# Kernel optimization log

Measured on AMD Instinct MI355X. Metric: run time of the kernel, lower is better.

Reference implementation:

```python
import jax, jax.numpy as jnp
import numpy as np

SEQ, BATCH, HID, OUT = 2048, 128, 256, 2

def setup_inputs() -> dict:
    key = jax.random.key(0)
    ks = jax.random.split(key, 6)
    return {
        "x": jax.random.normal(ks[0], (SEQ, BATCH), dtype=jnp.float32),
        # torch code draws h inside forward: randn*0.01 + 0.5 -> pass as input for determinism
        "h0": jax.random.normal(ks[1], (BATCH, HID), dtype=jnp.float32) * 0.01 + 0.5,
        "W_ih": jax.random.normal(ks[2], (HID, 1), dtype=jnp.float32) * 0.05 + 0.4,
        "W_hh": jax.random.normal(ks[3], (HID, HID), dtype=jnp.float32) * 0.2,
        "W_hh_bias": jax.random.normal(ks[4], (HID, HID), dtype=jnp.float32) * 0.01 + 0.5,
        "b_h": jnp.zeros((HID,), dtype=jnp.float32),
        "W": jax.random.normal(ks[5], (OUT, HID), dtype=jnp.float32) * 0.1 + 0.5,
        "b": jnp.zeros((OUT,), dtype=jnp.float32),
        "context": 1,
    }

def reference(x, h0, W_ih, W_hh, W_hh_bias, b_h, W, b, context):
    # context is a scalar, so c1 + c2 = (2h-1) @ (W_hh + context*W_hh_bias).T (same math, one GEMM)
    W_eff = W_hh + context * W_hh_bias            # (hid, hid)
    w_in = W_ih[:, 0]                             # input_size == 1 -> (hid,)

    def step(h, x_t):
        # c0: (batch,1)@(1,hid) == outer product of x_t with W_ih column
        pre = x_t[:, None] * w_in[None, :] + (2.0 * h - 1.0) @ W_eff.T + b_h
        h_new = jax.nn.sigmoid(pre)
        return h_new, h_new

    _, hs = jax.lax.scan(step, h0, x)             # hs: (seq, batch, hid)
    out = jnp.transpose(hs, (1, 0, 2))            # (batch, seq, hid)
    y = out @ W.T + b                             # (batch, seq, out)
    return y[:, :, 0], out
```

## Files before the change

kernel.cpp:

```cpp
#include <hip/hip_runtime.h>
#include <math.h>

#define SEQ   2048
#define BATCH 128
#define HID   256
#define NCH   16
#define KCH   16
#define VST   20

template <int CTRL>
__device__ __forceinline__ float dpp_mov(float x) {
    return __int_as_float(__builtin_amdgcn_update_dpp(
        __float_as_int(x), __float_as_int(x), CTRL, 0xF, 0xF, false));
}

__global__ __launch_bounds__(512, 2)
void rnn_scan_kernel(const float* __restrict__ x,
                     const float* __restrict__ h0,
                     const float* __restrict__ W_ih,
                     const float* __restrict__ W_hh,
                     const float* __restrict__ W_hh_b,
                     const float* __restrict__ b_h,
                     const int*   __restrict__ context,
                     float*       __restrict__ out_hs)
{
    const int b   = blockIdx.x;
    const int tid = threadIdx.x;
    const int R   = tid >> 4;
    const int l   = tid & 15;
    const int l7  = tid & 7;
    const int row = 8 * R + l7;

    __shared__ __align__(16) float v_lds[2][NCH * VST];
    __shared__ float x_lds[SEQ];

    for (int t = tid; t < SEQ; t += 512)
        x_lds[t] = x[t * BATCH + b];

    const float ctx = (float)context[0];

    float4 wreg[8][4];
    #pragma unroll
    for (int j = 0; j < 8; ++j) {
        const int rj = 8 * R + (l7 ^ j);
        const float* wp = W_hh   + (size_t)rj * HID + KCH * l;
        const float* bp = W_hh_b + (size_t)rj * HID + KCH * l;
        #pragma unroll
        for (int c = 0; c < 4; ++c) {
            const float4 a = *(const float4*)(wp + 4 * c);
            const float4 d = *(const float4*)(bp + 4 * c);
            wreg[j][c] = make_float4(a.x + ctx * d.x, a.y + ctx * d.y,
                                     a.z + ctx * d.z, a.w + ctx * d.w);
        }
    }

    const float winj = W_ih[row];
    const float bhj  = b_h[row];

    const int voff = VST * (row >> 4) + (row & 15);
    v_lds[0][voff] = 2.f * h0[(size_t)b * HID + row] - 1.f;

    float* outp = out_hs + (size_t)b * SEQ * HID + row;

    const float4* vr0 = (const float4*)(v_lds[0] + VST * l);
    const float4* vr1 = (const float4*)(v_lds[1] + VST * l);

    __syncthreads();

    auto step = [&](int t, const float4* __restrict__ vr, float* __restrict__ vw) {
        float q[8] = {0.f, 0.f, 0.f, 0.f, 0.f, 0.f, 0.f, 0.f};
        #pragma unroll
        for (int c = 0; c < 4; ++c) {
            const float4 v4 = vr[c];
            #pragma unroll
            for (int j = 0; j < 8; ++j) {
                const float4 w = wreg[j][c];
                q[j] += w.x * v4.x;
                q[j] += w.y * v4.y;
                q[j] += w.z * v4.z;
                q[j] += w.w * v4.w;
            }
        }
        #pragma unroll
        for (int j = 0; j < 8; ++j) q[j] += dpp_mov<0x128>(q[j]);
        q[0] += dpp_mov<0xB1>(q[1]);
        q[2] += dpp_mov<0xB1>(q[3]);
        q[4] += dpp_mov<0xB1>(q[5]);
        q[6] += dpp_mov<0xB1>(q[7]);
        q[0] += dpp_mov<0x4E>(q[2]);
        q[4] += dpp_mov<0x4E>(q[6]);
        q[0] += dpp_mov<0x124>(q[4]);

        const float pre = q[0] + bhj + x_lds[t] * winj;
        const float h = __builtin_amdgcn_rcpf(1.f + __expf(-pre));
        vw[voff] = 2.f * h - 1.f;
        if ((tid & 8) == 0)
            outp[(size_t)t * HID] = h;
        __syncthreads();
    };

    for (int t = 0; t < SEQ; t += 2) {
        step(t,     vr0, v_lds[1]);
        step(t + 1, vr1, v_lds[0]);
    }
}

__global__ __launch_bounds__(256, 4)
void head_kernel(const float* __restrict__ hs,
                 const float* __restrict__ W,
                 const float* __restrict__ bias,
                 float*       __restrict__ y)
{
    const int tid  = threadIdx.x;
    const int lane = tid & 63;
    const int sub  = lane & 15;
    const int rsub = lane >> 4;

    float4 w0[4];
    #pragma unroll
    for (int u = 0; u < 4; ++u)
        w0[u] = *(const float4*)(W + 4 * (16 * u + sub));
    const float b0 = bias[0];

    const int gwave = (blockIdx.x * blockDim.x + tid) >> 6;
    const int nw    = (gridDim.x * blockDim.x) >> 6;
    const int nq    = (BATCH * SEQ) >> 2;

    for (int q = gwave; q < nq; q += nw) {
        const int rrow = q * 4 + rsub;
        const float* rp = hs + (size_t)rrow * HID;
        float s = 0.f;
        #pragma unroll
        for (int u = 0; u < 4; ++u) {
            const float4 hv = *(const float4*)(rp + 4 * (16 * u + sub));
            s += hv.x * w0[u].x + hv.y * w0[u].y +
                 hv.z * w0[u].z + hv.w * w0[u].w;
        }
        s += __shfl_xor(s, 1, 64);
        s += __shfl_xor(s, 2, 64);
        s += __shfl_xor(s, 4, 64);
        s += __shfl_xor(s, 8, 64);
        if (sub == 0) y[rrow] = s + b0;
    }
}

extern "C" void kernel_launch(void* const* d_in, const int* in_sizes, int n_in,
                              void* d_out, int out_size, void* d_ws, size_t ws_size,
                              hipStream_t stream) {
    const float* x      = (const float*)d_in[0];
    const float* h0     = (const float*)d_in[1];
    const float* W_ih   = (const float*)d_in[2];
    const float* W_hh   = (const float*)d_in[3];
    const float* W_hh_b = (const float*)d_in[4];
    const float* b_h    = (const float*)d_in[5];
    const float* W      = (const float*)d_in[6];
    const float* bias   = (const float*)d_in[7];
    const int*   ctx    = (const int*)d_in[8];

    float* y  = (float*)d_out;
    float* hs = y + (size_t)BATCH * SEQ;

    rnn_scan_kernel<<<BATCH, 512, 0, stream>>>(x, h0, W_ih, W_hh, W_hh_b,
                                               b_h, ctx, hs);
    head_kernel<<<2048, 256, 0, stream>>>(hs, W, bias, y);
}
```

Before: 1.470 ms.

## Fuse output head projection into RNN scan kernel epilogue

Removes the separate head kernel and has each scan block compute y for its own batch row after the recurrence finishes, reading back the hs it just wrote. This drops one kernel launch and lets the head work run per block without a second grid. In exchange the head runs on only 128 blocks, so bandwidth use is lower, and it adds a threadfence. It also changes the sigmoid reciprocal from rcpf to a full divide, changes the launch-bounds attribute to waves_per_eu, and hoists the x_lds load to the top of the step.

```diff
diff --git a/kernel.cpp b/kernel.cpp
--- a/kernel.cpp
+++ b/kernel.cpp
@@ -14,7 +14,7 @@
         __float_as_int(x), __float_as_int(x), CTRL, 0xF, 0xF, false));
 }
 
-__global__ __launch_bounds__(512, 2)
+__global__ __launch_bounds__(512) __attribute__((amdgpu_waves_per_eu(2, 2)))
 void rnn_scan_kernel(const float* __restrict__ x,
                      const float* __restrict__ h0,
                      const float* __restrict__ W_ih,
@@ -22,7 +22,10 @@
                      const float* __restrict__ W_hh_b,
                      const float* __restrict__ b_h,
                      const int*   __restrict__ context,
-                     float*       __restrict__ out_hs)
+                     const float* __restrict__ Wout,
+                     const float* __restrict__ bias,
+                     float*       __restrict__ out_hs,
+                     float*       __restrict__ out_y)
 {
     const int b   = blockIdx.x;
     const int tid = threadIdx.x;
@@ -68,6 +71,7 @@
     __syncthreads();
 
     auto step = [&](int t, const float4* __restrict__ vr, float* __restrict__ vw) {
+        const float xt = x_lds[t];
         float q[8] = {0.f, 0.f, 0.f, 0.f, 0.f, 0.f, 0.f, 0.f};
         #pragma unroll
         for (int c = 0; c < 4; ++c) {
@@ -91,8 +95,8 @@
         q[4] += dpp_mov<0x4E>(q[6]);
         q[0] += dpp_mov<0x124>(q[4]);
 
-        const float pre = q[0] + bhj + x_lds[t] * winj;
-        const float h = __builtin_amdgcn_rcpf(1.f + __expf(-pre));
+        const float pre = q[0] + bhj + xt * winj;
+        const float h = 1.f / (1.f + __expf(-pre));
         vw[voff] = 2.f * h - 1.f;
         if ((tid & 8) == 0)
             outp[(size_t)t * HID] = h;
@@ -103,44 +107,37 @@
         step(t,     vr0, v_lds[1]);
         step(t + 1, vr1, v_lds[0]);
     }
-}
 
-__global__ __launch_bounds__(256, 4)
-void head_kernel(const float* __restrict__ hs,
-                 const float* __restrict__ W,
-                 const float* __restrict__ bias,
-                 float*       __restrict__ y)
-{
-    const int tid  = threadIdx.x;
-    const int lane = tid & 63;
-    const int sub  = lane & 15;
-    const int rsub = lane >> 4;
+    __threadfence();
+    __syncthreads();
 
-    float4 w0[4];
-    #pragma unroll
-    for (int u = 0; u < 4; ++u)
-        w0[u] = *(const float4*)(W + 4 * (16 * u + sub));
-    const float b0 = bias[0];
+    {
+        const int sub  = tid & 15;
+        const int rsub = tid >> 4;
+        float4 w0[4];
+        #pragma unroll
+        for (int u = 0; u < 4; ++u)
+            w0[u] = *(const float4*)(Wout + 4 * (16 * u + sub));
+        const float b0 = bias[0];
+        const float* hsb = out_hs + (size_t)b * SEQ * HID;
+        float* yp = out_y + (size_t)b * SEQ;
 
-    const int gwave = (blockIdx.x * blockDim.x + tid) >> 6;
-    const int nw    = (gridDim.x * blockDim.x) >> 6;
-    const int nq    = (BATCH * SEQ) >> 2;
-
-    for (int q = gwave; q < nq; q += nw) {
-        const int rrow = q * 4 + rsub;
-        const float* rp = hs + (size_t)rrow * HID;
-        float s = 0.f;
-        #pragma unroll
-        for (int u = 0; u < 4; ++u) {
-            const float4 hv = *(const float4*)(rp + 4 * (16 * u + sub));
-            s += hv.x * w0[u].x + hv.y * w0[u].y +
-                 hv.z * w0[u].z + hv.w * w0[u].w;
+        for (int r0 = 0; r0 < SEQ; r0 += 32) {
+            const int t = r0 + rsub;
+            const float* rp = hsb + (size_t)t * HID;
+            float s = 0.f;
+            #pragma unroll
+            for (int u = 0; u < 4; ++u) {
+                const float4 hv = *(const float4*)(rp + 4 * (16 * u + sub));
+                s += hv.x * w0[u].x + hv.y * w0[u].y +
+                     hv.z * w0[u].z + hv.w * w0[u].w;
+            }
+            s += __shfl_xor(s, 1, 64);
+            s += __shfl_xor(s, 2, 64);
+            s += __shfl_xor(s, 4, 64);
+            s += __shfl_xor(s, 8, 64);
+            if (sub == 0) yp[t] = s + b0;
         }
-        s += __shfl_xor(s, 1, 64);
-        s += __shfl_xor(s, 2, 64);
-        s += __shfl_xor(s, 4, 64);
-        s += __shfl_xor(s, 8, 64);
-        if (sub == 0) y[rrow] = s + b0;
     }
 }
 
@@ -161,6 +158,5 @@
     float* hs = y + (size_t)BATCH * SEQ;
 
     rnn_scan_kernel<<<BATCH, 512, 0, stream>>>(x, h0, W_ih, W_hh, W_hh_b,
-                                               b_h, ctx, hs);
-    head_kernel<<<2048, 256, 0, stream>>>(hs, W, bias, y);
+                                               b_h, ctx, W, bias, hs, y);
 }
```

Measured after the change: 1.404 ms. 4.6% less time.
